# Kernel optimization log

Hardware: AMD Instinct MI355X
Metric: run time of the kernel (lower is better)

Reference implementation:

```python
import jax, jax.numpy as jnp
import numpy as np

STATE_MASS = 4.0
EPS = 1e-5
LOW_RANK_SCALE = 0.1  # _LOW_RANK_SCALE_INIT


def _ln(x, g, b):
    mu = jnp.mean(x, axis=-1, keepdims=True)
    var = jnp.var(x, axis=-1, keepdims=True)
    return (x - mu) * jax.lax.rsqrt(var + EPS) * g + b


def _signed_abs_softmax(s, axis=-1):
    s = jnp.nan_to_num(s)
    return jnp.sign(s) * jax.nn.softmax(jnp.abs(s), axis=axis)


def _signed_softmax_state(st):
    st = jnp.nan_to_num(st)
    return jnp.sign(st) * jax.nn.softmax(jnp.abs(st), axis=-1) * STATE_MASS


def _low_rank_scores(dst, src, Ut_w, Ut_b, Us_w, Us_b, w):
    # bilinear low-rank pairwise: score[b,i,j] = sum_r (dst_i Ut)_r * w_r * (src_j Us)_r
    pt = dst @ Ut_w + Ut_b                      # [B,Nd,R]
    ps = src @ Us_w + Us_b                      # [B,Ns,R]
    return jnp.einsum('bir,r,bjr->bij', pt, w * LOW_RANK_SCALE, ps)


def _gather_rows(x, idx):
    # x: [B,N,...], idx: [B,M,K] -> [B,M,K,...] (per-batch gather, no NxM broadcast)
    return jax.vmap(lambda xi, ii: xi[ii])(x, idx)


def setup_inputs() -> dict:
    key = jax.random.key(0)
    ks = jax.random.split(key, 8)
    B, S, D, M, R = 16, 2048, 512, 256, 64
    std = 0.02
    return {
        'token_val': jax.random.normal(ks[0], (B, S, D), jnp.float32),
        'token_state': jax.random.normal(ks[1], (B, S), jnp.float32),
        'init_state': jax.random.normal(ks[2], (M,), jnp.float32) * std,
        'init_val': jax.random.normal(ks[3], (M, D), jnp.float32) * std,
        'rUs_w': jax.random.normal(ks[4], (D, R), jnp.float32) * std,
        'rUs_b': jnp.zeros((R,), jnp.float32),
        'rUt_w': jax.random.normal(ks[5], (D, R), jnp.float32) * std,
        'rUt_b': jnp.zeros((R,), jnp.float32),
        'r_w': jnp.ones((R,), jnp.float32),
        'pUs_w': jax.random.normal(ks[6], (D, R), jnp.float32) * std,
        'pUs_b': jnp.zeros((R,), jnp.float32),
        'pUt_w': jax.random.normal(ks[7], (D, R), jnp.float32) * std,
        'pUt_b': jnp.zeros((R,), jnp.float32),
        'p_w': jnp.ones((R,), jnp.float32),
        'ln_g': jnp.ones((D,), jnp.float32),
        'ln_b': jnp.zeros((D,), jnp.float32),
        'topk': 16,
    }


def reference(token_val, token_state, init_state, init_val,
              rUs_w, rUs_b, rUt_w, rUt_b, r_w,
              pUs_w, pUs_b, pUt_w, pUt_b, p_w,
              ln_g, ln_b, topk):
    B = token_val.shape[0]
    M, D = init_val.shape

    # _MemoryLevel.initialize
    mem_state = _signed_softmax_state(jnp.broadcast_to(init_state, (B, M)))
    mem_val = _ln(jnp.broadcast_to(init_val, (B, M, D)), ln_g, ln_b)

    # ---- SparseTransition (write): route tokens -> slots, top-k sources/slot ----
    scores = _low_rank_scores(mem_val, token_val, rUt_w, rUt_b, rUs_w, rUs_b, r_w)  # [B,M,S]
    _, idx = jax.lax.top_k(jnp.abs(scores), topk)              # [B,M,K]
    sel = jnp.take_along_axis(scores, idx, axis=-1)            # [B,M,K]
    edges = _signed_abs_softmax(sel, axis=-1)                  # signed-abs-softmax over edges
    v_sel = _gather_rows(token_val, idx)                       # [B,M,K,D]
    s_sel = _gather_rows(token_state, idx)                     # [B,M,K]
    mem_val = mem_val + jnp.einsum('bmk,bmkd->bmd', edges, v_sel)   # merge_mode='add'
    mem_state = mem_state + jnp.einsum('bmk,bmk->bm', edges, s_sel)
    mem_state = _signed_softmax_state(mem_state)
    mem_val = _ln(mem_val, ln_g, ln_b)

    # ---- SparsePropagation within slots: state-weighted top-k edges, residual ----
    pscores = _low_rank_scores(mem_val, mem_val, pUt_w, pUt_b, pUs_w, pUs_b, p_w)   # [B,M,M]
    pscores = pscores * mem_state[:, None, :]                  # state_weight_edges
    _, pidx = jax.lax.top_k(jnp.abs(pscores), topk)            # [B,M,K]
    psel = jnp.take_along_axis(pscores, pidx, axis=-1)
    pe = _signed_abs_softmax(psel, axis=-1)
    pv = _gather_rows(mem_val, pidx)                           # [B,M,K,D]
    pst = _gather_rows(mem_state, pidx)                        # [B,M,K]
    mem_val = mem_val + jnp.einsum('bmk,bmkd->bmd', pe, pv)    # residual=True
    mem_state = mem_state + jnp.einsum('bmk,bmk->bm', pe, pst)
    mem_state = _signed_softmax_state(mem_state)
    mem_val = _ln(mem_val, ln_g, ln_b)
    return mem_val
```

## Files before the change

kernel.cpp:

```cpp
#include <hip/hip_runtime.h>
#include <hip/hip_bf16.h>
#include <math.h>

#define BB 16
#define SS 2048
#define DD 512
#define MM 256
#define RR 64
#define KK 16
#define GPAD 68

__device__ __forceinline__ float wave_sum(float v) {
#pragma unroll
  for (int off = 32; off > 0; off >>= 1) v += __shfl_xor(v, off);
  return v;
}

__device__ __forceinline__ float sgnf(float v) {
  return (v > 0.f) ? 1.f : ((v < 0.f) ? -1.f : 0.f);
}

template <bool TRANS_OUT>
__device__ __forceinline__ void gemm_body(
    const float* __restrict__ A, const float* __restrict__ W,
    const float* __restrict__ bias, const float* __restrict__ colscale,
    float csmul, float* __restrict__ C, int row0, float (*Ast)[GPAD],
    float (*Ws)[GPAD]) {
  int tid = threadIdx.x;
  int ty = tid >> 4, tx = tid & 15;
  float acc[4][4] = {};
  for (int kc = 0; kc < DD; kc += 32) {
#pragma unroll
    for (int i = 0; i < 2; ++i) {
      int s4 = i * 256 + tid;
      int r = s4 >> 3;
      int k4 = s4 & 7;
      float4 v = *reinterpret_cast<const float4*>(
          &A[(size_t)(row0 + r) * DD + kc + k4 * 4]);
      Ast[k4 * 4 + 0][r] = v.x;
      Ast[k4 * 4 + 1][r] = v.y;
      Ast[k4 * 4 + 2][r] = v.z;
      Ast[k4 * 4 + 3][r] = v.w;
    }
#pragma unroll
    for (int i = 0; i < 2; ++i) {
      int s4 = i * 256 + tid;
      int r = s4 >> 4;
      int c4 = s4 & 15;
      float4 v = *reinterpret_cast<const float4*>(
          &W[(size_t)(kc + r) * RR + c4 * 4]);
      *reinterpret_cast<float4*>(&Ws[r][c4 * 4]) = v;
    }
    __syncthreads();
#pragma unroll
    for (int k = 0; k < 32; ++k) {
      float4 a4 = *reinterpret_cast<const float4*>(&Ast[k][ty * 4]);
      float4 w4 = *reinterpret_cast<const float4*>(&Ws[k][tx * 4]);
      acc[0][0] += a4.x * w4.x; acc[0][1] += a4.x * w4.y;
      acc[0][2] += a4.x * w4.z; acc[0][3] += a4.x * w4.w;
      acc[1][0] += a4.y * w4.x; acc[1][1] += a4.y * w4.y;
      acc[1][2] += a4.y * w4.z; acc[1][3] += a4.y * w4.w;
      acc[2][0] += a4.z * w4.x; acc[2][1] += a4.z * w4.y;
      acc[2][2] += a4.z * w4.z; acc[2][3] += a4.z * w4.w;
      acc[3][0] += a4.w * w4.x; acc[3][1] += a4.w * w4.y;
      acc[3][2] += a4.w * w4.z; acc[3][3] += a4.w * w4.w;
    }
    __syncthreads();
  }
#pragma unroll
  for (int i = 0; i < 4; ++i) {
    int rr = row0 + ty * 4 + i;
    if (TRANS_OUT) {
#pragma unroll
      for (int j = 0; j < 4; ++j) {
        int cc = tx * 4 + j;
        float v = acc[i][j] + bias[cc];
        if (colscale) v *= colscale[cc] * csmul;
        C[((size_t)(rr >> 8) * RR + cc) * MM + (rr & 255)] = v;
      }
    } else {
      float4 o;
      o.x = acc[i][0] + bias[tx * 4];
      o.y = acc[i][1] + bias[tx * 4 + 1];
      o.z = acc[i][2] + bias[tx * 4 + 2];
      o.w = acc[i][3] + bias[tx * 4 + 3];
      if (colscale) {
        o.x *= colscale[tx * 4] * csmul; o.y *= colscale[tx * 4 + 1] * csmul;
        o.z *= colscale[tx * 4 + 2] * csmul; o.w *= colscale[tx * 4 + 3] * csmul;
      }
      *reinterpret_cast<float4*>(&C[(size_t)rr * RR + tx * 4]) = o;
    }
  }
}

__global__ __launch_bounds__(256) void k_ps_init(
    const float* __restrict__ token_val, const float* __restrict__ rUs_w,
    const float* __restrict__ rUs_b, float* __restrict__ ps,
    const float* __restrict__ init_val, const float* __restrict__ init_state,
    const float* __restrict__ ln_g, const float* __restrict__ ln_b,
    const float* __restrict__ rUt_w, const float* __restrict__ rUt_b,
    const float* __restrict__ r_w, float* __restrict__ mv0,
    float* __restrict__ pt0, float* __restrict__ ms0) {
  __shared__ float Ast[32][GPAD];
  __shared__ float Ws[32][GPAD];
  int t = threadIdx.x;
  if (blockIdx.x < 512) {
    gemm_body<false>(token_val, rUs_w, rUs_b, nullptr, 1.f, ps,
                     blockIdx.x * 64, Ast, Ws);
    return;
  }
  int m = blockIdx.x - 512;
  float* row = &Ast[0][0];
  float* red = &Ws[0][0];
  float* part = &Ws[1][0];
  if (m == 0) {
    float v = init_state[t];
    float a = fabsf(v);
    float mx = a;
#pragma unroll
    for (int off = 32; off > 0; off >>= 1) mx = fmaxf(mx, __shfl_xor(mx, off));
    if ((t & 63) == 0) red[4 + (t >> 6)] = mx;
    __syncthreads();
    mx = fmaxf(fmaxf(red[4], red[5]), fmaxf(red[6], red[7]));
    __syncthreads();
    float e = expf(a - mx);
    float ssum = wave_sum(e);
    if ((t & 63) == 0) red[4 + (t >> 6)] = ssum;
    __syncthreads();
    ssum = red[4] + red[5] + red[6] + red[7];
    ms0[t] = sgnf(v) * e / ssum * 4.0f;
    __syncthreads();
  }
  float x0 = init_val[m * DD + t];
  float x1 = init_val[m * DD + t + 256];
  float s = wave_sum(x0 + x1);
  float sq = wave_sum(x0 * x0 + x1 * x1);
  __syncthreads();
  if ((t & 63) == 0) { red[t >> 6] = s; red[4 + (t >> 6)] = sq; }
  __syncthreads();
  float mean = (red[0] + red[1] + red[2] + red[3]) * (1.0f / DD);
  float var = (red[4] + red[5] + red[6] + red[7]) * (1.0f / DD) - mean * mean;
  float rs = rsqrtf(var + 1e-5f);
  float n0 = (x0 - mean) * rs * ln_g[t] + ln_b[t];
  float n1 = (x1 - mean) * rs * ln_g[t + 256] + ln_b[t + 256];
  mv0[m * DD + t] = n0;
  mv0[m * DD + t + 256] = n1;
  row[t] = n0;
  row[t + 256] = n1;
  __syncthreads();
  {
    int r = t & 63, q = t >> 6;
    float acc = 0.f;
    const float* wp = rUt_w + (size_t)(q * 128) * RR + r;
#pragma unroll 16
    for (int d = 0; d < 128; ++d) acc += row[q * 128 + d] * wp[d * RR];
    part[q * RR + r] = acc;
  }
  __syncthreads();
  if (t < RR) {
    float acc = part[t] + part[RR + t] + part[2 * RR + t] + part[3 * RR + t] +
                rUt_b[t];
    pt0[m * RR + t] = acc * r_w[t] * 0.1f;
  }
}

__global__ __launch_bounds__(256) void k_gemm_pair(
    const float* __restrict__ mv1, const float* __restrict__ pUt_w,
    const float* __restrict__ pUt_b, const float* __restrict__ p_w,
    const float* __restrict__ pUs_w, const float* __restrict__ pUs_b,
    float* __restrict__ pt1, float* __restrict__ ps1T) {
  __shared__ float Ast[32][GPAD];
  __shared__ float Ws[32][GPAD];
  if (blockIdx.x < 64) {
    gemm_body<false>(mv1, pUt_w, pUt_b, p_w, 0.1f, pt1, blockIdx.x * 64,
                     Ast, Ws);
  } else {
    gemm_body<true>(mv1, pUs_w, pUs_b, nullptr, 1.f, ps1T,
                    (blockIdx.x - 64) * 64, Ast, Ws);
  }
}

#define PSW 144
__device__ __forceinline__ int psw(int j) { return j + ((j >> 5) << 2); }

__global__ __launch_bounds__(256) void k_scores(
    const float* __restrict__ pt0, const float* __restrict__ ps,
    float* __restrict__ scores) {
  __shared__ float PtT[RR][128];
  __shared__ float PsT[RR][PSW];
  int t = threadIdx.x;
  int b = blockIdx.z;
  int m0 = blockIdx.y * 128;
  int j0 = blockIdx.x * 128;
#pragma unroll
  for (int ii = 0; ii < 2; ++ii) {
    int slot = ii * 256 + t;
    int tm4 = slot >> 4, tk4 = slot & 15;
    const float* base = pt0 + (size_t)(m0 + tm4 * 4) * RR + tk4 * 4;
    float4 v0 = *reinterpret_cast<const float4*>(base);
    float4 v1 = *reinterpret_cast<const float4*>(base + RR);
    float4 v2 = *reinterpret_cast<const float4*>(base + 2 * RR);
    float4 v3 = *reinterpret_cast<const float4*>(base + 3 * RR);
    float4 w;
    w.x = v0.x; w.y = v1.x; w.z = v2.x; w.w = v3.x;
    *reinterpret_cast<float4*>(&PtT[tk4 * 4 + 0][tm4 * 4]) = w;
    w.x = v0.y; w.y = v1.y; w.z = v2.y; w.w = v3.y;
    *reinterpret_cast<float4*>(&PtT[tk4 * 4 + 1][tm4 * 4]) = w;
    w.x = v0.z; w.y = v1.z; w.z = v2.z; w.w = v3.z;
    *reinterpret_cast<float4*>(&PtT[tk4 * 4 + 2][tm4 * 4]) = w;
    w.x = v0.w; w.y = v1.w; w.z = v2.w; w.w = v3.w;
    *reinterpret_cast<float4*>(&PtT[tk4 * 4 + 3][tm4 * 4]) = w;
  }
#pragma unroll
  for (int ii = 0; ii < 2; ++ii) {
    int slot = ii * 256 + t;
    int jt = slot >> 4, kt = slot & 15;
    const float* base = ps + ((size_t)b * SS + j0 + jt * 4) * RR + kt * 4;
    float4 v0 = *reinterpret_cast<const float4*>(base);
    float4 v1 = *reinterpret_cast<const float4*>(base + RR);
    float4 v2 = *reinterpret_cast<const float4*>(base + 2 * RR);
    float4 v3 = *reinterpret_cast<const float4*>(base + 3 * RR);
    int jc = psw(jt * 4);
    float4 w;
    w.x = v0.x; w.y = v1.x; w.z = v2.x; w.w = v3.x;
    *reinterpret_cast<float4*>(&PsT[kt * 4 + 0][jc]) = w;
    w.x = v0.y; w.y = v1.y; w.z = v2.y; w.w = v3.y;
    *reinterpret_cast<float4*>(&PsT[kt * 4 + 1][jc]) = w;
    w.x = v0.z; w.y = v1.z; w.z = v2.z; w.w = v3.z;
    *reinterpret_cast<float4*>(&PsT[kt * 4 + 2][jc]) = w;
    w.x = v0.w; w.y = v1.w; w.z = v2.w; w.w = v3.w;
    *reinterpret_cast<float4*>(&PsT[kt * 4 + 3][jc]) = w;
  }
  __syncthreads();
  int jg = t & 15;
  int mg = t >> 4;
  int jlo = psw(jg * 8);
  float acc[8][8] = {};
#pragma unroll
  for (int k = 0; k < RR; ++k) {
    float4 a0 = *reinterpret_cast<const float4*>(&PtT[k][mg * 8]);
    float4 a1 = *reinterpret_cast<const float4*>(&PtT[k][mg * 8 + 4]);
    float4 w0 = *reinterpret_cast<const float4*>(&PsT[k][jlo]);
    float4 w1 = *reinterpret_cast<const float4*>(&PsT[k][jlo + 4]);
    float av[8] = {a0.x, a0.y, a0.z, a0.w, a1.x, a1.y, a1.z, a1.w};
    float wv[8] = {w0.x, w0.y, w0.z, w0.w, w1.x, w1.y, w1.z, w1.w};
#pragma unroll
    for (int r = 0; r < 8; ++r)
#pragma unroll
      for (int cc = 0; cc < 8; ++cc) acc[r][cc] += av[r] * wv[cc];
  }
  float* obase =
      scores + (size_t)b * MM * SS + (size_t)(m0 + mg * 8) * SS + j0 + jg * 8;
#pragma unroll
  for (int r = 0; r < 8; ++r) {
    float4 o0, o1;
    o0.x = acc[r][0]; o0.y = acc[r][1]; o0.z = acc[r][2]; o0.w = acc[r][3];
    o1.x = acc[r][4]; o1.y = acc[r][5]; o1.z = acc[r][6]; o1.w = acc[r][7];
    *reinterpret_cast<float4*>(obase + (size_t)r * SS) = o0;
    *reinterpret_cast<float4*>(obase + (size_t)r * SS + 4) = o1;
  }
}

__global__ __launch_bounds__(256) void k_write(
    const float* __restrict__ scores, const float* __restrict__ token_val,
    const float* __restrict__ token_state, const float* __restrict__ mv0,
    const float* __restrict__ ms0, const float* __restrict__ ln_g,
    const float* __restrict__ ln_b, float* __restrict__ mv1,
    float* __restrict__ ms_w) {
  int t = threadIdx.x;
  int wave = t >> 6, lane = t & 63;
  int i = blockIdx.x;
  int slot = i >> 3;
  int b = 2 * (i & 7) + (slot >> 6);
  int m = (slot & 63) * 4 + wave;
  int row = b * MM + m;
  __shared__ int selj_sh[4][KK];
  const float* srow = scores + (size_t)row * SS;
  unsigned au[32];
  unsigned maxa = 0u;
#pragma unroll
  for (int ch = 0; ch < 8; ++ch) {
    float4 q = *reinterpret_cast<const float4*>(srow + (ch * 64 + lane) * 4);
    au[ch * 4 + 0] = __float_as_uint(q.x) & 0x7fffffffu;
    au[ch * 4 + 1] = __float_as_uint(q.y) & 0x7fffffffu;
    au[ch * 4 + 2] = __float_as_uint(q.z) & 0x7fffffffu;
    au[ch * 4 + 3] = __float_as_uint(q.w) & 0x7fffffffu;
    maxa = max(maxa, max(max(au[ch * 4], au[ch * 4 + 1]),
                         max(au[ch * 4 + 2], au[ch * 4 + 3])));
  }
#pragma unroll
  for (int off = 32; off > 0; off >>= 1)
    maxa = max(maxa, (unsigned)__shfl_xor((int)maxa, off));
  unsigned lo = 0u, hi = maxa, thr = 0u;
  bool early = false;
  while (lo < hi) {
    unsigned mid = lo + ((hi - lo + 1u) >> 1);
    int cnt = 0;
#pragma unroll
    for (int c = 0; c < 32; ++c) cnt += __popcll(__ballot(au[c] >= mid));
    if (cnt == KK) { thr = mid; early = true; break; }
    if (cnt > KK) lo = mid; else hi = mid - 1u;
  }
  if (!early) thr = lo;
  unsigned long long ltmask = (1ull << lane) - 1ull;
  int s = 0;
  unsigned tiemask = 0u;
#pragma unroll
  for (int c = 0; c < 32; ++c) {
    bool sg = early ? (au[c] >= thr) : (au[c] > thr);
    unsigned long long mk = __ballot(sg);
    if (sg)
      selj_sh[wave][s + __popcll(mk & ltmask)] =
          (c >> 2) * 256 + lane * 4 + (c & 3);
    s += __popcll(mk);
    if (!early && au[c] == thr) tiemask |= 1u << c;
  }
  int taken = s;
  while (taken < KK) {
    int myj = 0x7fffffff;
#pragma unroll
    for (int c = 0; c < 32; ++c)
      if ((tiemask >> c) & 1u) {
        int j = (c >> 2) * 256 + lane * 4 + (c & 3);
        myj = min(myj, j);
      }
    int wj = myj;
#pragma unroll
    for (int off = 32; off > 0; off >>= 1) wj = min(wj, __shfl_xor(wj, off));
    if (wj == 0x7fffffff) break;
    if (((wj >> 2) & 63) == lane) tiemask &= ~(1u << (((wj >> 8) << 2) | (wj & 3)));
    if (lane == 0) selj_sh[wave][taken] = wj;
    ++taken;
  }
  int js[KK];
  float es[KK];
#pragma unroll
  for (int k = 0; k < KK; ++k) {
    js[k] = selj_sh[wave][k];
    es[k] = srow[js[k]];
  }
  float mx = 0.f;
#pragma unroll
  for (int k = 0; k < KK; ++k) mx = fmaxf(mx, fabsf(es[k]));
  float ssum = 0.f;
#pragma unroll
  for (int k = 0; k < KK; ++k) {
    float ex = expf(fabsf(es[k]) - mx);
    ssum += ex;
    es[k] = sgnf(es[k]) * ex;
  }
  float inv = 1.f / ssum;
  int dbase = lane * 8;
  const float* m0row = mv0 + m * DD + dbase;
  float4 a0 = *reinterpret_cast<const float4*>(m0row);
  float4 a1 = *reinterpret_cast<const float4*>(m0row + 4);
  float acc[8] = {a0.x, a0.y, a0.z, a0.w, a1.x, a1.y, a1.z, a1.w};
  float stacc = 0.f;
#pragma unroll
  for (int k = 0; k < KK; ++k) {
    float e = es[k] * inv;
    const float* tv = token_val + ((size_t)b * SS + js[k]) * DD + dbase;
    float4 u0 = *reinterpret_cast<const float4*>(tv);
    float4 u1 = *reinterpret_cast<const float4*>(tv + 4);
    acc[0] += e * u0.x; acc[1] += e * u0.y; acc[2] += e * u0.z; acc[3] += e * u0.w;
    acc[4] += e * u1.x; acc[5] += e * u1.y; acc[6] += e * u1.z; acc[7] += e * u1.w;
    stacc += e * token_state[(size_t)b * SS + js[k]];
  }
  if (lane == 0) ms_w[row] = ms0[m] + stacc;
  float s1 = 0.f, s2 = 0.f;
#pragma unroll
  for (int c = 0; c < 8; ++c) { s1 += acc[c]; s2 += acc[c] * acc[c]; }
  s1 = wave_sum(s1);
  s2 = wave_sum(s2);
  float mean = s1 * (1.0f / DD);
  float var = s2 * (1.0f / DD) - mean * mean;
  float rs = rsqrtf(var + 1e-5f);
  float4 g0 = *reinterpret_cast<const float4*>(ln_g + dbase);
  float4 g1 = *reinterpret_cast<const float4*>(ln_g + dbase + 4);
  float4 b0v = *reinterpret_cast<const float4*>(ln_b + dbase);
  float4 b1v = *reinterpret_cast<const float4*>(ln_b + dbase + 4);
  float4 o0, o1;
  o0.x = (acc[0] - mean) * rs * g0.x + b0v.x;
  o0.y = (acc[1] - mean) * rs * g0.y + b0v.y;
  o0.z = (acc[2] - mean) * rs * g0.z + b0v.z;
  o0.w = (acc[3] - mean) * rs * g0.w + b0v.w;
  o1.x = (acc[4] - mean) * rs * g1.x + b1v.x;
  o1.y = (acc[5] - mean) * rs * g1.y + b1v.y;
  o1.z = (acc[6] - mean) * rs * g1.z + b1v.z;
  o1.w = (acc[7] - mean) * rs * g1.w + b1v.w;
  float* orow = mv1 + (size_t)row * DD + dbase;
  *reinterpret_cast<float4*>(orow) = o0;
  *reinterpret_cast<float4*>(orow + 4) = o1;
}

__global__ __launch_bounds__(256, 4) void k_prop(
    const float* __restrict__ pt1, const float* __restrict__ ps1T,
    const float* __restrict__ ms_w, const float* __restrict__ mv1,
    const float* __restrict__ ln_g, const float* __restrict__ ln_b,
    float* __restrict__ out) {
  int t = threadIdx.x;
  int wave = t >> 6, lane = t & 63;
  int row = blockIdx.x * 4 + wave;
  int b = row >> 8, m = row & 255;
  __shared__ int selj_sh[4][KK];
  __shared__ float selv_sh[4][KK];
  __shared__ float ms1_sh[MM];
  __shared__ float red[4];
  {
    float v = ms_w[b * MM + t];
    float a = fabsf(v);
    float mx = a;
#pragma unroll
    for (int off = 32; off > 0; off >>= 1) mx = fmaxf(mx, __shfl_xor(mx, off));
    if ((t & 63) == 0) red[t >> 6] = mx;
    __syncthreads();
    mx = fmaxf(fmaxf(red[0], red[1]), fmaxf(red[2], red[3]));
    __syncthreads();
    float e = expf(a - mx);
    float ssum = wave_sum(e);
    if ((t & 63) == 0) red[t >> 6] = ssum;
    __syncthreads();
    ssum = red[0] + red[1] + red[2] + red[3];
    ms1_sh[t] = sgnf(v) * e / ssum * 4.0f;
  }
  __syncthreads();
  float ptval = pt1[(size_t)row * RR + lane];
  const float* pB = ps1T + (size_t)b * RR * MM + lane * 4;
  float sc[4] = {0.f, 0.f, 0.f, 0.f};
#pragma unroll 8
  for (int r = 0; r < RR; ++r) {
    float w = __shfl(ptval, r);
    float4 pv = *reinterpret_cast<const float4*>(pB + r * MM);
    sc[0] += w * pv.x; sc[1] += w * pv.y; sc[2] += w * pv.z; sc[3] += w * pv.w;
  }
  int jbase = lane * 4;
#pragma unroll
  for (int c = 0; c < 4; ++c) sc[c] *= ms1_sh[jbase + c];
  unsigned au[4];
#pragma unroll
  for (int c = 0; c < 4; ++c) au[c] = __float_as_uint(sc[c]) & 0x7fffffffu;
  unsigned lo = 0u, hi = 0x7f800000u, thr = 0u;
  bool early = false;
  while (lo < hi) {
    unsigned mid = lo + ((hi - lo + 1u) >> 1);
    int cnt = 0;
#pragma unroll
    for (int c = 0; c < 4; ++c) cnt += __popcll(__ballot(au[c] >= mid));
    if (cnt == KK) { thr = mid; early = true; break; }
    if (cnt > KK) lo = mid; else hi = mid - 1u;
  }
  if (!early) thr = lo;
  unsigned long long ltmask = (1ull << lane) - 1ull;
  int s = 0;
  unsigned tiemask = 0u;
#pragma unroll
  for (int c = 0; c < 4; ++c) {
    bool sg = early ? (au[c] >= thr) : (au[c] > thr);
    unsigned long long mk = __ballot(sg);
    if (sg) {
      int slot = s + __popcll(mk & ltmask);
      selj_sh[wave][slot] = jbase + c;
      selv_sh[wave][slot] = sc[c];
    }
    s += __popcll(mk);
    if (!early && au[c] == thr) tiemask |= 1u << c;
  }
  int taken = s;
  while (taken < KK) {
    int myj = 0x7fffffff;
#pragma unroll
    for (int c = 0; c < 4; ++c)
      if ((tiemask >> c) & 1u) myj = min(myj, jbase + c);
    int wj = myj;
#pragma unroll
    for (int off = 32; off > 0; off >>= 1) wj = min(wj, __shfl_xor(wj, off));
    if (wj == 0x7fffffff) break;
    if (wj >= jbase && wj < jbase + 4) {
      tiemask &= ~(1u << (wj - jbase));
      selv_sh[wave][taken] = sc[wj - jbase];
      if (lane == (wj >> 2)) selj_sh[wave][taken] = wj;
    }
    ++taken;
  }
  int js[KK];
  float es[KK];
#pragma unroll
  for (int k = 0; k < KK; ++k) { js[k] = selj_sh[wave][k]; es[k] = selv_sh[wave][k]; }
  float mx = 0.f;
#pragma unroll
  for (int k = 0; k < KK; ++k) mx = fmaxf(mx, fabsf(es[k]));
  float ssum = 0.f;
#pragma unroll
  for (int k = 0; k < KK; ++k) {
    float ex = expf(fabsf(es[k]) - mx);
    ssum += ex;
    es[k] = sgnf(es[k]) * ex;
  }
  float inv = 1.f / ssum;
  int dbase = lane * 8;
  const float* mrow = mv1 + (size_t)row * DD + dbase;
  float4 a0 = *reinterpret_cast<const float4*>(mrow);
  float4 a1 = *reinterpret_cast<const float4*>(mrow + 4);
  float acc[8] = {a0.x, a0.y, a0.z, a0.w, a1.x, a1.y, a1.z, a1.w};
#pragma unroll
  for (int k = 0; k < KK; ++k) {
    float e = es[k] * inv;
    const float* pv = mv1 + ((size_t)b * MM + js[k]) * DD + dbase;
    float4 u0 = *reinterpret_cast<const float4*>(pv);
    float4 u1 = *reinterpret_cast<const float4*>(pv + 4);
    acc[0] += e * u0.x; acc[1] += e * u0.y; acc[2] += e * u0.z; acc[3] += e * u0.w;
    acc[4] += e * u1.x; acc[5] += e * u1.y; acc[6] += e * u1.z; acc[7] += e * u1.w;
  }
  float s1 = 0.f, s2 = 0.f;
#pragma unroll
  for (int c = 0; c < 8; ++c) { s1 += acc[c]; s2 += acc[c] * acc[c]; }
  s1 = wave_sum(s1);
  s2 = wave_sum(s2);
  float mean = s1 * (1.0f / DD);
  float var = s2 * (1.0f / DD) - mean * mean;
  float rs = rsqrtf(var + 1e-5f);
  float4 g0 = *reinterpret_cast<const float4*>(ln_g + dbase);
  float4 g1 = *reinterpret_cast<const float4*>(ln_g + dbase + 4);
  float4 b0v = *reinterpret_cast<const float4*>(ln_b + dbase);
  float4 b1v = *reinterpret_cast<const float4*>(ln_b + dbase + 4);
  float4 o0, o1;
  o0.x = (acc[0] - mean) * rs * g0.x + b0v.x;
  o0.y = (acc[1] - mean) * rs * g0.y + b0v.y;
  o0.z = (acc[2] - mean) * rs * g0.z + b0v.z;
  o0.w = (acc[3] - mean) * rs * g0.w + b0v.w;
  o1.x = (acc[4] - mean) * rs * g1.x + b1v.x;
  o1.y = (acc[5] - mean) * rs * g1.y + b1v.y;
  o1.z = (acc[6] - mean) * rs * g1.z + b1v.z;
  o1.w = (acc[7] - mean) * rs * g1.w + b1v.w;
  float* orow = out + (size_t)row * DD + dbase;
  *reinterpret_cast<float4*>(orow) = o0;
  *reinterpret_cast<float4*>(orow + 4) = o1;
}

extern "C" void kernel_launch(void* const* d_in, const int* in_sizes, int n_in,
                              void* d_out, int out_size, void* d_ws,
                              size_t ws_size, hipStream_t stream) {
  const float* token_val = (const float*)d_in[0];
  const float* token_state = (const float*)d_in[1];
  const float* init_state = (const float*)d_in[2];
  const float* init_val = (const float*)d_in[3];
  const float* rUs_w = (const float*)d_in[4];
  const float* rUs_b = (const float*)d_in[5];
  const float* rUt_w = (const float*)d_in[6];
  const float* rUt_b = (const float*)d_in[7];
  const float* r_w = (const float*)d_in[8];
  const float* pUs_w = (const float*)d_in[9];
  const float* pUs_b = (const float*)d_in[10];
  const float* pUt_w = (const float*)d_in[11];
  const float* pUt_b = (const float*)d_in[12];
  const float* p_w = (const float*)d_in[13];
  const float* ln_g = (const float*)d_in[14];
  const float* ln_b = (const float*)d_in[15];
  float* out = (float*)d_out;

  float* ws = (float*)d_ws;
  float* mv0 = ws;    ws += MM * DD;
  float* pt0 = ws;    ws += MM * RR;
  float* ms0 = ws;    ws += MM;
  float* ps = ws;     ws += (size_t)BB * SS * RR;
  float* scores = ws; ws += (size_t)BB * MM * SS;
  float* mv1 = ws;    ws += (size_t)BB * MM * DD;
  float* ms_w = ws;   ws += BB * MM;
  float* pt1 = ws;    ws += (size_t)BB * MM * RR;
  float* ps1T = ws;   ws += (size_t)BB * RR * MM;

  k_ps_init<<<768, 256, 0, stream>>>(token_val, rUs_w, rUs_b, ps, init_val,
                                     init_state, ln_g, ln_b, rUt_w, rUt_b,
                                     r_w, mv0, pt0, ms0);
  dim3 gs(SS / 128, MM / 128, BB);
  k_scores<<<gs, 256, 0, stream>>>(pt0, ps, scores);
  k_write<<<(BB * MM) / 4, 256, 0, stream>>>(scores, token_val, token_state,
                                             mv0, ms0, ln_g, ln_b, mv1, ms_w);
  k_gemm_pair<<<128, 256, 0, stream>>>(mv1, pUt_w, pUt_b, p_w, pUs_w, pUs_b,
                                       pt1, ps1T);
  k_prop<<<(BB * MM) / 4, 256, 0, stream>>>(pt1, ps1T, ms_w, mv1, ln_g, ln_b,
                                            out);
}
```

Baseline: 148.3 us.

## Split token projection GEMM over K halves with larger 128x64 tiles

```diff
diff --git a/kernel.cpp b/kernel.cpp
--- a/kernel.cpp
+++ b/kernel.cpp
@@ -9,6 +9,7 @@
 #define RR 64
 #define KK 16
 #define GPAD 68
+#define APAD 132
 
 __device__ __forceinline__ float wave_sum(float v) {
 #pragma unroll
@@ -20,18 +21,17 @@
   return (v > 0.f) ? 1.f : ((v < 0.f) ? -1.f : 0.f);
 }
 
-template <bool TRANS_OUT>
-__device__ __forceinline__ void gemm_body(
+__device__ __forceinline__ void gemm_ps_body(
     const float* __restrict__ A, const float* __restrict__ W,
-    const float* __restrict__ bias, const float* __restrict__ colscale,
-    float csmul, float* __restrict__ C, int row0, float (*Ast)[GPAD],
-    float (*Ws)[GPAD]) {
+    const float* __restrict__ bias, float* __restrict__ C, int row0, int k0,
+    bool addb, float (*Ast)[APAD], float (*Ws)[GPAD]) {
   int tid = threadIdx.x;
-  int ty = tid >> 4, tx = tid & 15;
-  float acc[4][4] = {};
-  for (int kc = 0; kc < DD; kc += 32) {
-#pragma unroll
-    for (int i = 0; i < 2; ++i) {
+  int ty = tid >> 3;
+  int tx = tid & 7;
+  float acc[4][8] = {};
+  for (int kc = k0; kc < k0 + 256; kc += 32) {
+#pragma unroll
+    for (int i = 0; i < 4; ++i) {
       int s4 = i * 256 + tid;
       int r = s4 >> 3;
       int k4 = s4 & 7;
@@ -55,58 +55,50 @@
 #pragma unroll
     for (int k = 0; k < 32; ++k) {
       float4 a4 = *reinterpret_cast<const float4*>(&Ast[k][ty * 4]);
-      float4 w4 = *reinterpret_cast<const float4*>(&Ws[k][tx * 4]);
-      acc[0][0] += a4.x * w4.x; acc[0][1] += a4.x * w4.y;
-      acc[0][2] += a4.x * w4.z; acc[0][3] += a4.x * w4.w;
-      acc[1][0] += a4.y * w4.x; acc[1][1] += a4.y * w4.y;
-      acc[1][2] += a4.y * w4.z; acc[1][3] += a4.y * w4.w;
-      acc[2][0] += a4.z * w4.x; acc[2][1] += a4.z * w4.y;
-      acc[2][2] += a4.z * w4.z; acc[2][3] += a4.z * w4.w;
-      acc[3][0] += a4.w * w4.x; acc[3][1] += a4.w * w4.y;
-      acc[3][2] += a4.w * w4.z; acc[3][3] += a4.w * w4.w;
-    }
-    __syncthreads();
-  }
+      float4 w0 = *reinterpret_cast<const float4*>(&Ws[k][tx * 8]);
+      float4 w1 = *reinterpret_cast<const float4*>(&Ws[k][tx * 8 + 4]);
+      float av[4] = {a4.x, a4.y, a4.z, a4.w};
+      float wv[8] = {w0.x, w0.y, w0.z, w0.w, w1.x, w1.y, w1.z, w1.w};
+#pragma unroll
+      for (int i = 0; i < 4; ++i)
+#pragma unroll
+        for (int j = 0; j < 8; ++j) acc[i][j] += av[i] * wv[j];
+    }
+    __syncthreads();
+  }
+  float bv[8];
+#pragma unroll
+  for (int j = 0; j < 8; ++j) bv[j] = addb ? bias[tx * 8 + j] : 0.f;
 #pragma unroll
   for (int i = 0; i < 4; ++i) {
     int rr = row0 + ty * 4 + i;
-    if (TRANS_OUT) {
-#pragma unroll
-      for (int j = 0; j < 4; ++j) {
-        int cc = tx * 4 + j;
-        float v = acc[i][j] + bias[cc];
-        if (colscale) v *= colscale[cc] * csmul;
-        C[((size_t)(rr >> 8) * RR + cc) * MM + (rr & 255)] = v;
-      }
-    } else {
-      float4 o;
-      o.x = acc[i][0] + bias[tx * 4];
-      o.y = acc[i][1] + bias[tx * 4 + 1];
-      o.z = acc[i][2] + bias[tx * 4 + 2];
-      o.w = acc[i][3] + bias[tx * 4 + 3];
-      if (colscale) {
-        o.x *= colscale[tx * 4] * csmul; o.y *= colscale[tx * 4 + 1] * csmul;
-        o.z *= colscale[tx * 4 + 2] * csmul; o.w *= colscale[tx * 4 + 3] * csmul;
-      }
-      *reinterpret_cast<float4*>(&C[(size_t)rr * RR + tx * 4]) = o;
-    }
+    float4 o0, o1;
+    o0.x = acc[i][0] + bv[0]; o0.y = acc[i][1] + bv[1];
+    o0.z = acc[i][2] + bv[2]; o0.w = acc[i][3] + bv[3];
+    o1.x = acc[i][4] + bv[4]; o1.y = acc[i][5] + bv[5];
+    o1.z = acc[i][6] + bv[6]; o1.w = acc[i][7] + bv[7];
+    *reinterpret_cast<float4*>(&C[(size_t)rr * RR + tx * 8]) = o0;
+    *reinterpret_cast<float4*>(&C[(size_t)rr * RR + tx * 8 + 4]) = o1;
   }
 }
 
 __global__ __launch_bounds__(256) void k_ps_init(
     const float* __restrict__ token_val, const float* __restrict__ rUs_w,
-    const float* __restrict__ rUs_b, float* __restrict__ ps,
-    const float* __restrict__ init_val, const float* __restrict__ init_state,
-    const float* __restrict__ ln_g, const float* __restrict__ ln_b,
-    const float* __restrict__ rUt_w, const float* __restrict__ rUt_b,
-    const float* __restrict__ r_w, float* __restrict__ mv0,
-    float* __restrict__ pt0, float* __restrict__ ms0) {
-  __shared__ float Ast[32][GPAD];
+    const float* __restrict__ rUs_b, float* __restrict__ ps0,
+    float* __restrict__ ps1, const float* __restrict__ init_val,
+    const float* __restrict__ init_state, const float* __restrict__ ln_g,
+    const float* __restrict__ ln_b, const float* __restrict__ rUt_w,
+    const float* __restrict__ rUt_b, const float* __restrict__ r_w,
+    float* __restrict__ mv0, float* __restrict__ pt0,
+    float* __restrict__ ms0) {
+  __shared__ float Ast[32][APAD];
   __shared__ float Ws[32][GPAD];
   int t = threadIdx.x;
   if (blockIdx.x < 512) {
-    gemm_body<false>(token_val, rUs_w, rUs_b, nullptr, 1.f, ps,
-                     blockIdx.x * 64, Ast, Ws);
+    int half = blockIdx.x >> 8;
+    int row0 = (blockIdx.x & 255) * 128;
+    gemm_ps_body(token_val, rUs_w, rUs_b, half ? ps1 : ps0, row0, half * 256,
+                 half == 0, Ast, Ws);
     return;
   }
   int m = blockIdx.x - 512;
@@ -164,6 +156,79 @@
   }
 }
 
+template <bool TRANS_OUT>
+__device__ __forceinline__ void gemm_body(
+    const float* __restrict__ A, const float* __restrict__ W,
+    const float* __restrict__ bias, const float* __restrict__ colscale,
+    float csmul, float* __restrict__ C, int row0, float (*Ast)[GPAD],
+    float (*Ws)[GPAD]) {
+  int tid = threadIdx.x;
+  int ty = tid >> 4, tx = tid & 15;
+  float acc[4][4] = {};
+  for (int kc = 0; kc < DD; kc += 32) {
+#pragma unroll
+    for (int i = 0; i < 2; ++i) {
+      int s4 = i * 256 + tid;
+      int r = s4 >> 3;
+      int k4 = s4 & 7;
+      float4 v = *reinterpret_cast<const float4*>(
+          &A[(size_t)(row0 + r) * DD + kc + k4 * 4]);
+      Ast[k4 * 4 + 0][r] = v.x;
+      Ast[k4 * 4 + 1][r] = v.y;
+      Ast[k4 * 4 + 2][r] = v.z;
+      Ast[k4 * 4 + 3][r] = v.w;
+    }
+#pragma unroll
+    for (int i = 0; i < 2; ++i) {
+      int s4 = i * 256 + tid;
+      int r = s4 >> 4;
+      int c4 = s4 & 15;
+      float4 v = *reinterpret_cast<const float4*>(
+          &W[(size_t)(kc + r) * RR + c4 * 4]);
+      *reinterpret_cast<float4*>(&Ws[r][c4 * 4]) = v;
+    }
+    __syncthreads();
+#pragma unroll
+    for (int k = 0; k < 32; ++k) {
+      float4 a4 = *reinterpret_cast<const float4*>(&Ast[k][ty * 4]);
+      float4 w4 = *reinterpret_cast<const float4*>(&Ws[k][tx * 4]);
+      acc[0][0] += a4.x * w4.x; acc[0][1] += a4.x * w4.y;
+      acc[0][2] += a4.x * w4.z; acc[0][3] += a4.x * w4.w;
+      acc[1][0] += a4.y * w4.x; acc[1][1] += a4.y * w4.y;
+      acc[1][2] += a4.y * w4.z; acc[1][3] += a4.y * w4.w;
+      acc[2][0] += a4.z * w4.x; acc[2][1] += a4.z * w4.y;
+      acc[2][2] += a4.z * w4.z; acc[2][3] += a4.z * w4.w;
+      acc[3][0] += a4.w * w4.x; acc[3][1] += a4.w * w4.y;
+      acc[3][2] += a4.w * w4.z; acc[3][3] += a4.w * w4.w;
+    }
+    __syncthreads();
+  }
+#pragma unroll
+  for (int i = 0; i < 4; ++i) {
+    int rr = row0 + ty * 4 + i;
+    if (TRANS_OUT) {
+#pragma unroll
+      for (int j = 0; j < 4; ++j) {
+        int cc = tx * 4 + j;
+        float v = acc[i][j] + bias[cc];
+        if (colscale) v *= colscale[cc] * csmul;
+        C[((size_t)(rr >> 8) * RR + cc) * MM + (rr & 255)] = v;
+      }
+    } else {
+      float4 o;
+      o.x = acc[i][0] + bias[tx * 4];
+      o.y = acc[i][1] + bias[tx * 4 + 1];
+      o.z = acc[i][2] + bias[tx * 4 + 2];
+      o.w = acc[i][3] + bias[tx * 4 + 3];
+      if (colscale) {
+        o.x *= colscale[tx * 4] * csmul; o.y *= colscale[tx * 4 + 1] * csmul;
+        o.z *= colscale[tx * 4 + 2] * csmul; o.w *= colscale[tx * 4 + 3] * csmul;
+      }
+      *reinterpret_cast<float4*>(&C[(size_t)rr * RR + tx * 4]) = o;
+    }
+  }
+}
+
 __global__ __launch_bounds__(256) void k_gemm_pair(
     const float* __restrict__ mv1, const float* __restrict__ pUt_w,
     const float* __restrict__ pUt_b, const float* __restrict__ p_w,
@@ -184,8 +249,8 @@
 __device__ __forceinline__ int psw(int j) { return j + ((j >> 5) << 2); }
 
 __global__ __launch_bounds__(256) void k_scores(
-    const float* __restrict__ pt0, const float* __restrict__ ps,
-    float* __restrict__ scores) {
+    const float* __restrict__ pt0, const float* __restrict__ ps0,
+    const float* __restrict__ ps1, float* __restrict__ scores) {
   __shared__ float PtT[RR][128];
   __shared__ float PsT[RR][PSW];
   int t = threadIdx.x;
@@ -215,11 +280,21 @@
   for (int ii = 0; ii < 2; ++ii) {
     int slot = ii * 256 + t;
     int jt = slot >> 4, kt = slot & 15;
-    const float* base = ps + ((size_t)b * SS + j0 + jt * 4) * RR + kt * 4;
-    float4 v0 = *reinterpret_cast<const float4*>(base);
-    float4 v1 = *reinterpret_cast<const float4*>(base + RR);
-    float4 v2 = *reinterpret_cast<const float4*>(base + 2 * RR);
-    float4 v3 = *reinterpret_cast<const float4*>(base + 3 * RR);
+    size_t off = ((size_t)b * SS + j0 + jt * 4) * RR + kt * 4;
+    const float* base0 = ps0 + off;
+    const float* base1 = ps1 + off;
+    float4 v0 = *reinterpret_cast<const float4*>(base0);
+    float4 v1 = *reinterpret_cast<const float4*>(base0 + RR);
+    float4 v2 = *reinterpret_cast<const float4*>(base0 + 2 * RR);
+    float4 v3 = *reinterpret_cast<const float4*>(base0 + 3 * RR);
+    float4 u0 = *reinterpret_cast<const float4*>(base1);
+    float4 u1 = *reinterpret_cast<const float4*>(base1 + RR);
+    float4 u2 = *reinterpret_cast<const float4*>(base1 + 2 * RR);
+    float4 u3 = *reinterpret_cast<const float4*>(base1 + 3 * RR);
+    v0.x += u0.x; v0.y += u0.y; v0.z += u0.z; v0.w += u0.w;
+    v1.x += u1.x; v1.y += u1.y; v1.z += u1.z; v1.w += u1.w;
+    v2.x += u2.x; v2.y += u2.y; v2.z += u2.z; v2.w += u2.w;
+    v3.x += u3.x; v3.y += u3.y; v3.z += u3.z; v3.w += u3.w;
     int jc = psw(jt * 4);
     float4 w;
     w.x = v0.x; w.y = v1.x; w.z = v2.x; w.w = v3.x;
@@ -568,12 +643,13 @@
   float* ms_w = ws;   ws += BB * MM;
   float* pt1 = ws;    ws += (size_t)BB * MM * RR;
   float* ps1T = ws;   ws += (size_t)BB * RR * MM;
-
-  k_ps_init<<<768, 256, 0, stream>>>(token_val, rUs_w, rUs_b, ps, init_val,
-                                     init_state, ln_g, ln_b, rUt_w, rUt_b,
-                                     r_w, mv0, pt0, ms0);
+  float* psB = mv1;
+
+  k_ps_init<<<768, 256, 0, stream>>>(token_val, rUs_w, rUs_b, ps, psB,
+                                     init_val, init_state, ln_g, ln_b, rUt_w,
+                                     rUt_b, r_w, mv0, pt0, ms0);
   dim3 gs(SS / 128, MM / 128, BB);
-  k_scores<<<gs, 256, 0, stream>>>(pt0, ps, scores);
+  k_scores<<<gs, 256, 0, stream>>>(pt0, ps, psB, scores);
   k_write<<<(BB * MM) / 4, 256, 0, stream>>>(scores, token_val, token_state,
                                              mv0, ms0, ln_g, ln_b, mv1, ms_w);
   k_gemm_pair<<<128, 256, 0, stream>>>(mv1, pUt_w, pUt_b, p_w, pUs_w, pUs_b,
```

After: 150.1 us. Within noise of the previous version (+1.2%).
